# Kernel tuning notes

Measured on AMD Instinct MI355X. Metric: run time of the kernel, lower is better.

## Reference

```python
import jax, jax.numpy as jnp
import numpy as np
import math

D_MODEL = 768
N_HEADS = 12
HEAD_DIM = D_MODEL // N_HEADS
B, T = 2, 4096


def setup_inputs() -> dict:
    key = jax.random.key(0)
    k1, k2, k3, k4 = jax.random.split(key, 4)
    x = jax.random.normal(k1, (B, T, D_MODEL), dtype=jnp.float32)
    mask = jax.random.randint(k2, (B, T), 0, 2).astype(jnp.bool_)
    # torch Linear init scale ~ 1/sqrt(fan_in); use scaled normal for stability
    w_qkv = jax.random.normal(k3, (3 * D_MODEL, D_MODEL), dtype=jnp.float32) / math.sqrt(D_MODEL)
    w_proj = jax.random.normal(k4, (D_MODEL, D_MODEL), dtype=jnp.float32) / math.sqrt(D_MODEL)
    b_proj = jnp.zeros((D_MODEL,), dtype=jnp.float32)
    return {"x": x, "mask": mask, "w_qkv": w_qkv, "w_proj": w_proj, "b_proj": b_proj}


def reference(x, mask, w_qkv, w_proj, b_proj):
    Bb, Tt, D = x.shape
    H, Hd = N_HEADS, HEAD_DIM
    scale = math.sqrt(Hd)
    # qkv projection (bias-free): (B,T,3D) -> (3,B,H,T,Hd)
    qkv = jnp.einsum('btd,ed->bte', x, w_qkv)
    qkv = qkv.reshape(Bb, Tt, 3, H, Hd).transpose(2, 0, 3, 1, 4)
    q, k, v = qkv[0], qkv[1], qkv[2]
    # full T x T scores (faithful to non-fused original)
    attn = jnp.einsum('bhqd,bhkd->bhqk', q, k) / scale
    attn = jnp.where(mask[:, None, None, :], -jnp.inf, attn)
    attn = jax.nn.softmax(attn, axis=-1)  # dropout p=0 -> identity
    out = jnp.einsum('bhqk,bhkd->bhqd', attn, v)
    out = out.transpose(0, 2, 1, 3).reshape(Bb, Tt, D)
    return jnp.einsum('btd,ed->bte', out, w_proj) + b_proj
```

## Files before the change

### kernel.cpp

```cpp
#include <hip/hip_runtime.h>

#define D_MODEL 768
#define N_HEADS 12
#define SEQ 4096
#define KVB 64

typedef __attribute__((ext_vector_type(4))) float f32x4;
typedef __attribute__((ext_vector_type(16))) float f32x16;
typedef __attribute__((ext_vector_type(8))) short bf16x8;
typedef __attribute__((ext_vector_type(4))) unsigned short u16x4;

typedef __attribute__((address_space(3))) void lds_void;
typedef __attribute__((address_space(1))) const void glb_void;

static __device__ __forceinline__ void gld_lds16(const void* g, void* l) {
    __builtin_amdgcn_global_load_lds((glb_void*)g, (lds_void*)l, 16, 0, 0);
}

static __device__ __forceinline__ unsigned short f32_bf16(float f) {
    union { float f; unsigned int u; } c; c.f = f;
    unsigned int u = c.u;
    u += 0x7FFFu + ((u >> 16) & 1u);
    return (unsigned short)(u >> 16);
}

static __device__ __forceinline__ unsigned int cvtpk(float lo, float hi) {
    unsigned int r;
    asm("v_cvt_pk_bf16_f32 %0, %1, %2" : "=v"(r) : "v"(lo), "v"(hi));
    return r;
}

__global__ void cvt_bf16(const float* __restrict__ in, unsigned short* __restrict__ out, int n) {
    int i = (blockIdx.x * blockDim.x + threadIdx.x) * 4;
    int stride = gridDim.x * blockDim.x * 4;
    for (; i < n; i += stride) {
        f32x4 v = *(const f32x4*)(in + i);
        u16x4 o;
        o[0] = f32_bf16(v[0]); o[1] = f32_bf16(v[1]);
        o[2] = f32_bf16(v[2]); o[3] = f32_bf16(v[3]);
        *(u16x4*)(out + i) = o;
    }
}

#define QSCL 0.18033688f

__global__ __launch_bounds__(256) void qkv_gemm(const unsigned short* __restrict__ A,
                                                const unsigned short* __restrict__ Bw,
                                                unsigned short* __restrict__ qb,
                                                unsigned short* __restrict__ kb,
                                                unsigned short* __restrict__ vb) {
    __shared__ __attribute__((aligned(16))) unsigned short lA[128*32];
    __shared__ __attribute__((aligned(16))) unsigned short lB[128*32];
    const int K = 768;
    int tid = threadIdx.x;
    int wave = tid >> 6, lane = tid & 63;
    int qr = (wave >> 1) * 64, qc = (wave & 1) * 64;
    int m0 = blockIdx.x * 128, n0 = blockIdx.y * 128;
    f32x4 acc[4][4] = {};
    const int sl = (((lane >> 4) ^ (lane & 3)) * 16);

    for (int kt = 0; kt < K; kt += 32) {
        __syncthreads();
        #pragma unroll
        for (int i = 0; i < 2; ++i) {
            int c = i*256 + tid;
            int row = c >> 2;
            int col = ((c & 3) ^ (row & 3)) * 8;
            char* dA = (char*)lA + (i*256 + wave*64)*16;
            char* dB = (char*)lB + (i*256 + wave*64)*16;
            gld_lds16(A  + (size_t)(m0 + row) * K + kt + col, dA);
            gld_lds16(Bw + (size_t)(n0 + row) * K + kt + col, dB);
        }
        __syncthreads();
        bf16x8 af[4], bfr[4];
        #pragma unroll
        for (int m = 0; m < 4; ++m)
            af[m] = *(bf16x8*)((char*)lA + (qr + m*16 + (lane & 15))*64 + sl);
        #pragma unroll
        for (int n = 0; n < 4; ++n)
            bfr[n] = *(bf16x8*)((char*)lB + (qc + n*16 + (lane & 15))*64 + sl);
        #pragma unroll
        for (int m = 0; m < 4; ++m)
            #pragma unroll
            for (int n = 0; n < 4; ++n)
                acc[m][n] = __builtin_amdgcn_mfma_f32_16x16x32_bf16(af[m], bfr[n], acc[m][n], 0, 0, 0);
    }
    #pragma unroll
    for (int n = 0; n < 4; ++n) {
        int colg = n0 + qc + n*16 + (lane & 15);
        int s = colg / 768;
        int rem = colg - s * 768;
        int h = rem >> 6, d = rem & 63;
        if (s == 2) {
            #pragma unroll
            for (int m = 0; m < 4; ++m) {
                int rowb = m0 + qr + m*16 + (lane >> 4)*4;
                int bb = rowb >> 12, t0 = rowb & 4095;
                int t0p = (t0 & ~12) | ((t0 & 4) << 1) | ((t0 & 8) >> 1);
                u16x4 pk;
                #pragma unroll
                for (int r = 0; r < 4; ++r) pk[r] = f32_bf16(acc[m][n][r]);
                *(u16x4*)(vb + ((size_t)((bb*12 + h)*64 + d))*4096 + t0p) = pk;
            }
        } else {
            unsigned short* dst = (s == 0) ? qb : kb;
            float scl = (s == 0) ? QSCL : 1.0f;
            #pragma unroll
            for (int m = 0; m < 4; ++m) {
                int rowb = m0 + qr + m*16 + (lane >> 4)*4;
                #pragma unroll
                for (int r = 0; r < 4; ++r) {
                    int row = rowb + r;
                    int bb = row >> 12, t = row & 4095;
                    dst[((size_t)((bb*12 + h)*4096 + t))*64 + d] = f32_bf16(acc[m][n][r] * scl);
                }
            }
        }
    }
}

__global__ __launch_bounds__(512, 4) void attn_kern(const unsigned short* __restrict__ qbuf,
                                                    const unsigned short* __restrict__ kbuf,
                                                    const unsigned short* __restrict__ vtbuf,
                                                    const int* __restrict__ mask,
                                                    unsigned short* __restrict__ ob) {
    __shared__ __attribute__((aligned(16))) char lds[3][16384];
    __shared__ float lds_l[4][32];

    const int tid = threadIdx.x, wave = tid >> 6, lane = tid & 63;
    const int l31 = lane & 31, hi2 = lane >> 5;
    const int lane16 = lane * 16;
    const int wq = wave & 3, wk = wave >> 2;

    int raw = blockIdx.x;
    int sb = (raw & 7) * 96 + (raw >> 3);
    int bh = sb >> 5, qi = sb & 31;
    int q0 = qi * 128;
    int b = bh / 12, h = bh - b*12;

    const unsigned short* Qb = qbuf + (size_t)bh * SEQ * 64;
    const unsigned short* Kb = kbuf + (size_t)bh * SEQ * 64;
    const unsigned short* Vt = vtbuf + (size_t)bh * 64 * SEQ;
    const int* mrow = mask + b * SEQ + wk*32 + l31;

    bf16x8 bq[4];
    #pragma unroll
    for (int ds = 0; ds < 4; ++ds)
        bq[ds] = *(const bf16x8*)(Qb + (size_t)(q0 + wq*32 + l31)*64 + ds*16 + hi2*8);
    __builtin_amdgcn_sched_barrier(0);

    union U4 { unsigned int w[4]; bf16x8 v; };
    U4 bext; bext.w[0] = (hi2 == 0) ? 0x3F80u : 0u; bext.w[1] = bext.w[2] = bext.w[3] = 0u;

    auto stage = [&](char* buf, int kv0) {
        #pragma unroll
        for (int i = 0; i < 2; ++i) {
            int fi = wave*2 + i;
            const unsigned short* gsrc;
            if (fi < 8) {
                int kt = fi >> 2, ds = fi & 3;
                gsrc = Kb + (size_t)(kv0 + kt*32 + l31)*64 + ds*16 + hi2*8;
            } else {
                int g = fi - 8, dt = g >> 2, ks = g & 3;
                gsrc = Vt + (size_t)(dt*32 + l31)*4096 + kv0 + ks*16 + hi2*8;
            }
            gld_lds16(gsrc, buf + fi*1024);
        }
    };

    f32x16 oacc0 = {}, oacc1 = {};
    float lr = 0.0f;

    char* bA = lds[0];
    char* bB = lds[1];
    char* bC = lds[2];

    stage(bA, 0);
    int mb0 = mrow[0];
    stage(bB, KVB);
    int mb1 = mrow[KVB];
    asm volatile("s_waitcnt vmcnt(3)" ::: "memory");
    __builtin_amdgcn_sched_barrier(0);
    __builtin_amdgcn_s_barrier();
    __builtin_amdgcn_sched_barrier(0);

    const int NT = SEQ / KVB;
    for (int t = 0; t < NT; ++t) {
        int mb2 = 0;
        if (t + 2 < NT) {
            stage(bC, (t + 2) * KVB);
            mb2 = mrow[(t + 2) * KVB];
        }
        char* bufK = bA;
        char* bufV = bA + 8192;

        U4 ab;
        ab.w[0] = (hi2 == 0) ? (mb0 ? 0xC480u : 0xC18Au) : 0u;
        ab.w[1] = ab.w[2] = ab.w[3] = 0u;

        f32x16 s = {};
        s = __builtin_amdgcn_mfma_f32_32x32x16_bf16(ab.v, bext.v, s, 0, 0, 0);
        #pragma unroll
        for (int ds = 0; ds < 4; ++ds) {
            bf16x8 aK = *(bf16x8*)(bufK + (wk*4 + ds)*1024 + lane16);
            s = __builtin_amdgcn_mfma_f32_32x32x16_bf16(aK, bq[ds], s, 0, 0, 0);
        }

        float rs = 0.0f;
        #pragma unroll
        for (int i = 0; i < 16; ++i) { s[i] = __builtin_amdgcn_exp2f(s[i]); rs += s[i]; }
        rs += __shfl_xor(rs, 32);
        lr += rs;

        bf16x8 pa[2];
        #pragma unroll
        for (int ks = 0; ks < 2; ++ks) {
            U4 w;
            w.w[0] = cvtpk(s[8*ks+0], s[8*ks+1]);
            w.w[1] = cvtpk(s[8*ks+2], s[8*ks+3]);
            w.w[2] = cvtpk(s[8*ks+4], s[8*ks+5]);
            w.w[3] = cvtpk(s[8*ks+6], s[8*ks+7]);
            pa[ks] = w.v;
        }

        #pragma unroll
        for (int sb2 = 0; sb2 < 2; ++sb2) {
            int ksg = wk*2 + sb2;
            bf16x8 bv0 = *(bf16x8*)(bufV + (0*4 + ksg)*1024 + lane16);
            bf16x8 bv1 = *(bf16x8*)(bufV + (1*4 + ksg)*1024 + lane16);
            oacc0 = __builtin_amdgcn_mfma_f32_32x32x16_bf16(pa[sb2], bv0, oacc0, 0, 0, 0);
            oacc1 = __builtin_amdgcn_mfma_f32_32x32x16_bf16(pa[sb2], bv1, oacc1, 0, 0, 0);
        }

        if (t + 2 < NT) {
            asm volatile("s_waitcnt vmcnt(3)" ::: "memory");
        } else {
            asm volatile("s_waitcnt vmcnt(0)" ::: "memory");
        }
        __builtin_amdgcn_sched_barrier(0);
        __builtin_amdgcn_s_barrier();
        __builtin_amdgcn_sched_barrier(0);

        char* tmp = bA; bA = bB; bB = bC; bC = tmp;
        mb0 = mb1; mb1 = mb2;
    }

    float* cbase = (float*)lds + wq * 2048;
    if (wk == 1) {
        #pragma unroll
        for (int i = 0; i < 16; ++i) {
            cbase[i*64 + lane]        = oacc0[i];
            cbase[(16 + i)*64 + lane] = oacc1[i];
        }
        if (lane < 32) lds_l[wq][lane] = lr;
    }
    __syncthreads();
    if (wk == 0 && lane < 32) lds_l[wq][lane] += lr;
    __syncthreads();
    if (wk == 0) {
        #pragma unroll
        for (int r = 0; r < 16; ++r) {
            int q = (r & 3) + 8*(r >> 2) + 4*hi2;
            float inv = 1.0f / lds_l[wq][q];
            int tg = q0 + wq*32 + q;
            size_t base = ((size_t)(b*SEQ + tg)) * D_MODEL + h*64 + l31;
            ob[base]      = f32_bf16((oacc0[r] + cbase[r*64 + lane])        * inv);
            ob[base + 32] = f32_bf16((oacc1[r] + cbase[(16 + r)*64 + lane]) * inv);
        }
    }
}

__global__ __launch_bounds__(256) void proj_gemm(const unsigned short* __restrict__ A,
                                                 const unsigned short* __restrict__ Bw,
                                                 const float* __restrict__ bias,
                                                 float* __restrict__ out) {
    __shared__ __attribute__((aligned(16))) unsigned short lA[128*32];
    __shared__ __attribute__((aligned(16))) unsigned short lB[128*32];
    const int K = 768;
    int tid = threadIdx.x;
    int wave = tid >> 6, lane = tid & 63;
    int qr = (wave >> 1) * 64, qc = (wave & 1) * 64;
    int m0 = blockIdx.x * 128, n0 = blockIdx.y * 128;
    f32x4 acc[4][4] = {};
    const int sl = (((lane >> 4) ^ (lane & 3)) * 16);

    for (int kt = 0; kt < K; kt += 32) {
        __syncthreads();
        #pragma unroll
        for (int i = 0; i < 2; ++i) {
            int c = i*256 + tid;
            int row = c >> 2;
            int col = ((c & 3) ^ (row & 3)) * 8;
            char* dA = (char*)lA + (i*256 + wave*64)*16;
            char* dB = (char*)lB + (i*256 + wave*64)*16;
            gld_lds16(A  + (size_t)(m0 + row) * K + kt + col, dA);
            gld_lds16(Bw + (size_t)(n0 + row) * K + kt + col, dB);
        }
        __syncthreads();
        bf16x8 af[4], bfr[4];
        #pragma unroll
        for (int m = 0; m < 4; ++m)
            af[m] = *(bf16x8*)((char*)lA + (qr + m*16 + (lane & 15))*64 + sl);
        #pragma unroll
        for (int n = 0; n < 4; ++n)
            bfr[n] = *(bf16x8*)((char*)lB + (qc + n*16 + (lane & 15))*64 + sl);
        #pragma unroll
        for (int m = 0; m < 4; ++m)
            #pragma unroll
            for (int n = 0; n < 4; ++n)
                acc[m][n] = __builtin_amdgcn_mfma_f32_16x16x32_bf16(af[m], bfr[n], acc[m][n], 0, 0, 0);
    }
    #pragma unroll
    for (int n = 0; n < 4; ++n) {
        int colg = n0 + qc + n*16 + (lane & 15);
        float bn = bias[colg];
        #pragma unroll
        for (int m = 0; m < 4; ++m) {
            int rowb = m0 + qr + m*16 + (lane >> 4)*4;
            #pragma unroll
            for (int r = 0; r < 4; ++r)
                out[(size_t)(rowb + r) * 768 + colg] = acc[m][n][r] + bn;
        }
    }
}

extern "C" void kernel_launch(void* const* d_in, const int* in_sizes, int n_in,
                              void* d_out, int out_size, void* d_ws, size_t ws_size,
                              hipStream_t stream) {
    const float* x      = (const float*)d_in[0];
    const int*   mask   = (const int*)d_in[1];
    const float* w_qkv  = (const float*)d_in[2];
    const float* w_proj = (const float*)d_in[3];
    const float* b_proj = (const float*)d_in[4];
    float* out = (float*)d_out;

    unsigned short* ws = (unsigned short*)d_ws;
    unsigned short* xb     = ws;
    unsigned short* wqkvb  = xb     + 6291456;
    unsigned short* wprojb = wqkvb  + 1769472;
    unsigned short* qb     = wprojb + 589824;
    unsigned short* kb     = qb     + 6291456;
    unsigned short* vtb    = kb     + 6291456;
    unsigned short* ob     = vtb    + 6291456;

    cvt_bf16<<<1024, 256, 0, stream>>>(x,      xb,     6291456);
    cvt_bf16<<<256,  256, 0, stream>>>(w_qkv,  wqkvb,  1769472);
    cvt_bf16<<<128,  256, 0, stream>>>(w_proj, wprojb, 589824);

    qkv_gemm<<<dim3(64, 18), 256, 0, stream>>>(xb, wqkvb, qb, kb, vtb);
    attn_kern<<<768, 512, 0, stream>>>(qb, kb, vtb, mask, ob);
    proj_gemm<<<dim3(64, 6), 256, 0, stream>>>(ob, wprojb, b_proj, out);
}
```

Baseline: 239.3 us.

## Halve attention block waves, each wave processes two query tiles sharing K/V fragments

The attention kernel now runs 4 waves per block instead of 8. Each wave computes two 32-row query tiles, so every K and V fragment read from LDS feeds two MFMAs and LDS read traffic per unit of work is halved. The K/V staging pipeline goes from triple to double buffering with a full vmcnt(0) wait each iteration. Register pressure doubles (four output accumulators, two score tiles), and with only one tile prefetched ahead, load latency may be less well hidden.

```diff
diff --git a/kernel.cpp b/kernel.cpp
--- a/kernel.cpp
+++ b/kernel.cpp
@@ -119,18 +119,18 @@
     }
 }
 
-__global__ __launch_bounds__(512, 4) void attn_kern(const unsigned short* __restrict__ qbuf,
+__global__ __launch_bounds__(256, 2) void attn_kern(const unsigned short* __restrict__ qbuf,
                                                     const unsigned short* __restrict__ kbuf,
                                                     const unsigned short* __restrict__ vtbuf,
                                                     const int* __restrict__ mask,
                                                     unsigned short* __restrict__ ob) {
-    __shared__ __attribute__((aligned(16))) char lds[3][16384];
-    __shared__ float lds_l[4][32];
+    __shared__ __attribute__((aligned(16))) char lds[2][16384];
+    __shared__ float lds_l[2][2][32];
 
     const int tid = threadIdx.x, wave = tid >> 6, lane = tid & 63;
     const int l31 = lane & 31, hi2 = lane >> 5;
     const int lane16 = lane * 16;
-    const int wq = wave & 3, wk = wave >> 2;
+    const int wq = wave & 1, wk = wave >> 1;
 
     int raw = blockIdx.x;
     int sb = (raw & 7) * 96 + (raw >> 3);
@@ -143,10 +143,12 @@
     const unsigned short* Vt = vtbuf + (size_t)bh * 64 * SEQ;
     const int* mrow = mask + b * SEQ + wk*32 + l31;
 
-    bf16x8 bq[4];
+    bf16x8 bqA[4], bqB[4];
     #pragma unroll
-    for (int ds = 0; ds < 4; ++ds)
-        bq[ds] = *(const bf16x8*)(Qb + (size_t)(q0 + wq*32 + l31)*64 + ds*16 + hi2*8);
+    for (int ds = 0; ds < 4; ++ds) {
+        bqA[ds] = *(const bf16x8*)(Qb + (size_t)(q0 + wq*64 + l31)*64      + ds*16 + hi2*8);
+        bqB[ds] = *(const bf16x8*)(Qb + (size_t)(q0 + wq*64 + 32 + l31)*64 + ds*16 + hi2*8);
+    }
     __builtin_amdgcn_sched_barrier(0);
 
     union U4 { unsigned int w[4]; bf16x8 v; };
@@ -154,8 +156,8 @@
 
     auto stage = [&](char* buf, int kv0) {
         #pragma unroll
-        for (int i = 0; i < 2; ++i) {
-            int fi = wave*2 + i;
+        for (int i = 0; i < 4; ++i) {
+            int fi = wave*4 + i;
             const unsigned short* gsrc;
             if (fi < 8) {
                 int kt = fi >> 2, ds = fi & 3;
@@ -168,104 +170,127 @@
         }
     };
 
-    f32x16 oacc0 = {}, oacc1 = {};
-    float lr = 0.0f;
+    f32x16 accA0 = {}, accA1 = {}, accB0 = {}, accB1 = {};
+    float lrA = 0.0f, lrB = 0.0f;
 
     char* bA = lds[0];
     char* bB = lds[1];
-    char* bC = lds[2];
 
     stage(bA, 0);
     int mb0 = mrow[0];
-    stage(bB, KVB);
-    int mb1 = mrow[KVB];
-    asm volatile("s_waitcnt vmcnt(3)" ::: "memory");
+    asm volatile("s_waitcnt vmcnt(0)" ::: "memory");
     __builtin_amdgcn_sched_barrier(0);
     __builtin_amdgcn_s_barrier();
     __builtin_amdgcn_sched_barrier(0);
 
     const int NT = SEQ / KVB;
     for (int t = 0; t < NT; ++t) {
-        int mb2 = 0;
-        if (t + 2 < NT) {
-            stage(bC, (t + 2) * KVB);
-            mb2 = mrow[(t + 2) * KVB];
-        }
-        char* bufK = bA;
-        char* bufV = bA + 8192;
+        int mb1 = 0;
+        if (t + 1 < NT) {
+            stage(bB, (t + 1) * KVB);
+            mb1 = mrow[(t + 1) * KVB];
+        }
+        const char* bufK = bA;
+        const char* bufV = bA + 8192;
+
+        bf16x8 kf0 = *(const bf16x8*)(bufK + (wk*4 + 0)*1024 + lane16);
+        bf16x8 kf1 = *(const bf16x8*)(bufK + (wk*4 + 1)*1024 + lane16);
+        bf16x8 kf2 = *(const bf16x8*)(bufK + (wk*4 + 2)*1024 + lane16);
+        bf16x8 kf3 = *(const bf16x8*)(bufK + (wk*4 + 3)*1024 + lane16);
 
         U4 ab;
         ab.w[0] = (hi2 == 0) ? (mb0 ? 0xC480u : 0xC18Au) : 0u;
         ab.w[1] = ab.w[2] = ab.w[3] = 0u;
 
-        f32x16 s = {};
-        s = __builtin_amdgcn_mfma_f32_32x32x16_bf16(ab.v, bext.v, s, 0, 0, 0);
-        #pragma unroll
-        for (int ds = 0; ds < 4; ++ds) {
-            bf16x8 aK = *(bf16x8*)(bufK + (wk*4 + ds)*1024 + lane16);
-            s = __builtin_amdgcn_mfma_f32_32x32x16_bf16(aK, bq[ds], s, 0, 0, 0);
-        }
-
-        float rs = 0.0f;
-        #pragma unroll
-        for (int i = 0; i < 16; ++i) { s[i] = __builtin_amdgcn_exp2f(s[i]); rs += s[i]; }
-        rs += __shfl_xor(rs, 32);
-        lr += rs;
-
-        bf16x8 pa[2];
-        #pragma unroll
-        for (int ks = 0; ks < 2; ++ks) {
-            U4 w;
-            w.w[0] = cvtpk(s[8*ks+0], s[8*ks+1]);
-            w.w[1] = cvtpk(s[8*ks+2], s[8*ks+3]);
-            w.w[2] = cvtpk(s[8*ks+4], s[8*ks+5]);
-            w.w[3] = cvtpk(s[8*ks+6], s[8*ks+7]);
-            pa[ks] = w.v;
-        }
-
-        #pragma unroll
-        for (int sb2 = 0; sb2 < 2; ++sb2) {
-            int ksg = wk*2 + sb2;
-            bf16x8 bv0 = *(bf16x8*)(bufV + (0*4 + ksg)*1024 + lane16);
-            bf16x8 bv1 = *(bf16x8*)(bufV + (1*4 + ksg)*1024 + lane16);
-            oacc0 = __builtin_amdgcn_mfma_f32_32x32x16_bf16(pa[sb2], bv0, oacc0, 0, 0, 0);
-            oacc1 = __builtin_amdgcn_mfma_f32_32x32x16_bf16(pa[sb2], bv1, oacc1, 0, 0, 0);
-        }
-
-        if (t + 2 < NT) {
-            asm volatile("s_waitcnt vmcnt(3)" ::: "memory");
-        } else {
-            asm volatile("s_waitcnt vmcnt(0)" ::: "memory");
-        }
+        f32x16 sA = {}, sB = {};
+        sA = __builtin_amdgcn_mfma_f32_32x32x16_bf16(ab.v, bext.v, sA, 0, 0, 0);
+        sB = __builtin_amdgcn_mfma_f32_32x32x16_bf16(ab.v, bext.v, sB, 0, 0, 0);
+        sA = __builtin_amdgcn_mfma_f32_32x32x16_bf16(kf0, bqA[0], sA, 0, 0, 0);
+        sB = __builtin_amdgcn_mfma_f32_32x32x16_bf16(kf0, bqB[0], sB, 0, 0, 0);
+        sA = __builtin_amdgcn_mfma_f32_32x32x16_bf16(kf1, bqA[1], sA, 0, 0, 0);
+        sB = __builtin_amdgcn_mfma_f32_32x32x16_bf16(kf1, bqB[1], sB, 0, 0, 0);
+        sA = __builtin_amdgcn_mfma_f32_32x32x16_bf16(kf2, bqA[2], sA, 0, 0, 0);
+        sB = __builtin_amdgcn_mfma_f32_32x32x16_bf16(kf2, bqB[2], sB, 0, 0, 0);
+        sA = __builtin_amdgcn_mfma_f32_32x32x16_bf16(kf3, bqA[3], sA, 0, 0, 0);
+        sB = __builtin_amdgcn_mfma_f32_32x32x16_bf16(kf3, bqB[3], sB, 0, 0, 0);
+
+        bf16x8 vf00 = *(const bf16x8*)(bufV + (0*4 + wk*2 + 0)*1024 + lane16);
+        bf16x8 vf10 = *(const bf16x8*)(bufV + (1*4 + wk*2 + 0)*1024 + lane16);
+        bf16x8 vf01 = *(const bf16x8*)(bufV + (0*4 + wk*2 + 1)*1024 + lane16);
+        bf16x8 vf11 = *(const bf16x8*)(bufV + (1*4 + wk*2 + 1)*1024 + lane16);
+
+        {
+            float rs = 0.0f;
+            #pragma unroll
+            for (int i = 0; i < 16; ++i) { sA[i] = __builtin_amdgcn_exp2f(sA[i]); rs += sA[i]; }
+            rs += __shfl_xor(rs, 32);
+            lrA += rs;
+            U4 p0, p1;
+            p0.w[0] = cvtpk(sA[0], sA[1]);  p0.w[1] = cvtpk(sA[2], sA[3]);
+            p0.w[2] = cvtpk(sA[4], sA[5]);  p0.w[3] = cvtpk(sA[6], sA[7]);
+            p1.w[0] = cvtpk(sA[8], sA[9]);  p1.w[1] = cvtpk(sA[10], sA[11]);
+            p1.w[2] = cvtpk(sA[12], sA[13]); p1.w[3] = cvtpk(sA[14], sA[15]);
+            accA0 = __builtin_amdgcn_mfma_f32_32x32x16_bf16(p0.v, vf00, accA0, 0, 0, 0);
+            accA1 = __builtin_amdgcn_mfma_f32_32x32x16_bf16(p0.v, vf10, accA1, 0, 0, 0);
+            accA0 = __builtin_amdgcn_mfma_f32_32x32x16_bf16(p1.v, vf01, accA0, 0, 0, 0);
+            accA1 = __builtin_amdgcn_mfma_f32_32x32x16_bf16(p1.v, vf11, accA1, 0, 0, 0);
+        }
+        {
+            float rs = 0.0f;
+            #pragma unroll
+            for (int i = 0; i < 16; ++i) { sB[i] = __builtin_amdgcn_exp2f(sB[i]); rs += sB[i]; }
+            rs += __shfl_xor(rs, 32);
+            lrB += rs;
+            U4 p0, p1;
+            p0.w[0] = cvtpk(sB[0], sB[1]);  p0.w[1] = cvtpk(sB[2], sB[3]);
+            p0.w[2] = cvtpk(sB[4], sB[5]);  p0.w[3] = cvtpk(sB[6], sB[7]);
+            p1.w[0] = cvtpk(sB[8], sB[9]);  p1.w[1] = cvtpk(sB[10], sB[11]);
+            p1.w[2] = cvtpk(sB[12], sB[13]); p1.w[3] = cvtpk(sB[14], sB[15]);
+            accB0 = __builtin_amdgcn_mfma_f32_32x32x16_bf16(p0.v, vf00, accB0, 0, 0, 0);
+            accB1 = __builtin_amdgcn_mfma_f32_32x32x16_bf16(p0.v, vf10, accB1, 0, 0, 0);
+            accB0 = __builtin_amdgcn_mfma_f32_32x32x16_bf16(p1.v, vf01, accB0, 0, 0, 0);
+            accB1 = __builtin_amdgcn_mfma_f32_32x32x16_bf16(p1.v, vf11, accB1, 0, 0, 0);
+        }
+
+        asm volatile("s_waitcnt vmcnt(0)" ::: "memory");
         __builtin_amdgcn_sched_barrier(0);
         __builtin_amdgcn_s_barrier();
         __builtin_amdgcn_sched_barrier(0);
 
-        char* tmp = bA; bA = bB; bB = bC; bC = tmp;
-        mb0 = mb1; mb1 = mb2;
-    }
-
-    float* cbase = (float*)lds + wq * 2048;
+        char* tmp = bA; bA = bB; bB = tmp;
+        mb0 = mb1;
+    }
+
+    float* cbase = (float*)lds + wq * 4096;
     if (wk == 1) {
         #pragma unroll
         for (int i = 0; i < 16; ++i) {
-            cbase[i*64 + lane]        = oacc0[i];
-            cbase[(16 + i)*64 + lane] = oacc1[i];
-        }
-        if (lane < 32) lds_l[wq][lane] = lr;
+            cbase[(     i)*64 + lane] = accA0[i];
+            cbase[(16 + i)*64 + lane] = accA1[i];
+            cbase[(32 + i)*64 + lane] = accB0[i];
+            cbase[(48 + i)*64 + lane] = accB1[i];
+        }
+        if (lane < 32) { lds_l[wq][0][lane] = lrA; lds_l[wq][1][lane] = lrB; }
     }
     __syncthreads();
-    if (wk == 0 && lane < 32) lds_l[wq][lane] += lr;
+    if (wk == 0 && lane < 32) {
+        lds_l[wq][0][lane] += lrA;
+        lds_l[wq][1][lane] += lrB;
+    }
     __syncthreads();
     if (wk == 0) {
         #pragma unroll
         for (int r = 0; r < 16; ++r) {
             int q = (r & 3) + 8*(r >> 2) + 4*hi2;
-            float inv = 1.0f / lds_l[wq][q];
-            int tg = q0 + wq*32 + q;
-            size_t base = ((size_t)(b*SEQ + tg)) * D_MODEL + h*64 + l31;
-            ob[base]      = f32_bf16((oacc0[r] + cbase[r*64 + lane])        * inv);
-            ob[base + 32] = f32_bf16((oacc1[r] + cbase[(16 + r)*64 + lane]) * inv);
+            float invA = 1.0f / lds_l[wq][0][q];
+            float invB = 1.0f / lds_l[wq][1][q];
+            int tA = q0 + wq*64 + q;
+            size_t baseA = ((size_t)(b*SEQ + tA)) * D_MODEL + h*64 + l31;
+            size_t baseB = baseA + (size_t)32 * D_MODEL;
+            ob[baseA]      = f32_bf16((accA0[r] + cbase[(     r)*64 + lane]) * invA);
+            ob[baseA + 32] = f32_bf16((accA1[r] + cbase[(16 + r)*64 + lane]) * invA);
+            ob[baseB]      = f32_bf16((accB0[r] + cbase[(32 + r)*64 + lane]) * invB);
+            ob[baseB + 32] = f32_bf16((accB1[r] + cbase[(48 + r)*64 + lane]) * invB);
         }
     }
 }
@@ -348,6 +373,6 @@
     cvt_bf16<<<128,  256, 0, stream>>>(w_proj, wprojb, 589824);
 
     qkv_gemm<<<dim3(64, 18), 256, 0, stream>>>(xb, wqkvb, qb, kb, vtb);
-    attn_kern<<<768, 512, 0, stream>>>(qb, kb, vtb, mask, ob);
+    attn_kern<<<768, 256, 0, stream>>>(qb, kb, vtb, mask, ob);
     proj_gemm<<<dim3(64, 6), 256, 0, stream>>>(ob, wprojb, b_proj, out);
 }
```

Result: faster. 230.8 us (-3.6%).

## Double KV block to 128 with two-stage double buffering in attention

Applied to the files above, without the earlier changes.

Raises the KV tile size from 64 to 128 keys and switches from a triple-buffered ring with one-ahead-by-two prefetch to double buffering, so each barrier covers twice as much MFMA work and the loop runs half as many iterations. Each wave now computes two 32-key score tiles per iteration with independent accumulator chains, which gives the scheduler more parallel work. The cost is a full vmcnt(0) wait each iteration, since prefetch depth drops to one tile. It also keeps LDS at 64KB per block, which may affect occupancy alongside extra registers for the second score tile.

```diff
diff --git a/kernel.cpp b/kernel.cpp
--- a/kernel.cpp
+++ b/kernel.cpp
@@ -3,7 +3,7 @@
 #define D_MODEL 768
 #define N_HEADS 12
 #define SEQ 4096
-#define KVB 64
+#define KVB 128
 
 typedef __attribute__((ext_vector_type(4))) float f32x4;
 typedef __attribute__((ext_vector_type(16))) float f32x16;
@@ -124,7 +124,7 @@
                                                     const unsigned short* __restrict__ vtbuf,
                                                     const int* __restrict__ mask,
                                                     unsigned short* __restrict__ ob) {
-    __shared__ __attribute__((aligned(16))) char lds[3][16384];
+    __shared__ __attribute__((aligned(16))) char lds[2][32768];
     __shared__ float lds_l[4][32];
 
     const int tid = threadIdx.x, wave = tid >> 6, lane = tid & 63;
@@ -141,7 +141,7 @@
     const unsigned short* Qb = qbuf + (size_t)bh * SEQ * 64;
     const unsigned short* Kb = kbuf + (size_t)bh * SEQ * 64;
     const unsigned short* Vt = vtbuf + (size_t)bh * 64 * SEQ;
-    const int* mrow = mask + b * SEQ + wk*32 + l31;
+    const int* mrow = mask + b * SEQ + wk*64 + l31;
 
     bf16x8 bq[4];
     #pragma unroll
@@ -154,14 +154,14 @@
 
     auto stage = [&](char* buf, int kv0) {
         #pragma unroll
-        for (int i = 0; i < 2; ++i) {
-            int fi = wave*2 + i;
+        for (int i = 0; i < 4; ++i) {
+            int fi = wave*4 + i;
             const unsigned short* gsrc;
-            if (fi < 8) {
+            if (fi < 16) {
                 int kt = fi >> 2, ds = fi & 3;
                 gsrc = Kb + (size_t)(kv0 + kt*32 + l31)*64 + ds*16 + hi2*8;
             } else {
-                int g = fi - 8, dt = g >> 2, ks = g & 3;
+                int g = fi - 16, dt = g >> 3, ks = g & 7;
                 gsrc = Vt + (size_t)(dt*32 + l31)*4096 + kv0 + ks*16 + hi2*8;
             }
             gld_lds16(gsrc, buf + fi*1024);
@@ -173,76 +173,93 @@
 
     char* bA = lds[0];
     char* bB = lds[1];
-    char* bC = lds[2];
 
     stage(bA, 0);
-    int mb0 = mrow[0];
-    stage(bB, KVB);
-    int mb1 = mrow[KVB];
-    asm volatile("s_waitcnt vmcnt(3)" ::: "memory");
+    int mbl0 = mrow[0], mbh0 = mrow[32];
+    asm volatile("s_waitcnt vmcnt(0)" ::: "memory");
     __builtin_amdgcn_sched_barrier(0);
     __builtin_amdgcn_s_barrier();
     __builtin_amdgcn_sched_barrier(0);
 
     const int NT = SEQ / KVB;
     for (int t = 0; t < NT; ++t) {
-        int mb2 = 0;
-        if (t + 2 < NT) {
-            stage(bC, (t + 2) * KVB);
-            mb2 = mrow[(t + 2) * KVB];
-        }
-        char* bufK = bA;
-        char* bufV = bA + 8192;
-
-        U4 ab;
-        ab.w[0] = (hi2 == 0) ? (mb0 ? 0xC480u : 0xC18Au) : 0u;
-        ab.w[1] = ab.w[2] = ab.w[3] = 0u;
-
-        f32x16 s = {};
-        s = __builtin_amdgcn_mfma_f32_32x32x16_bf16(ab.v, bext.v, s, 0, 0, 0);
+        int mbl1 = 0, mbh1 = 0;
+        if (t + 1 < NT) {
+            stage(bB, (t + 1) * KVB);
+            mbl1 = mrow[(t + 1) * KVB];
+            mbh1 = mrow[(t + 1) * KVB + 32];
+        }
+        const char* bufK = bA;
+        const char* bufV = bA + 16384;
+        const int kt0 = wk*2, kt1 = wk*2 + 1;
+
+        U4 ab0, ab1;
+        ab0.w[0] = (hi2 == 0) ? (mbl0 ? 0xC480u : 0xC18Au) : 0u;
+        ab0.w[1] = ab0.w[2] = ab0.w[3] = 0u;
+        ab1.w[0] = (hi2 == 0) ? (mbh0 ? 0xC480u : 0xC18Au) : 0u;
+        ab1.w[1] = ab1.w[2] = ab1.w[3] = 0u;
+
+        f32x16 s0 = {}, s1 = {};
+        s0 = __builtin_amdgcn_mfma_f32_32x32x16_bf16(ab0.v, bext.v, s0, 0, 0, 0);
+        s1 = __builtin_amdgcn_mfma_f32_32x32x16_bf16(ab1.v, bext.v, s1, 0, 0, 0);
         #pragma unroll
         for (int ds = 0; ds < 4; ++ds) {
-            bf16x8 aK = *(bf16x8*)(bufK + (wk*4 + ds)*1024 + lane16);
-            s = __builtin_amdgcn_mfma_f32_32x32x16_bf16(aK, bq[ds], s, 0, 0, 0);
-        }
-
-        float rs = 0.0f;
-        #pragma unroll
-        for (int i = 0; i < 16; ++i) { s[i] = __builtin_amdgcn_exp2f(s[i]); rs += s[i]; }
-        rs += __shfl_xor(rs, 32);
-        lr += rs;
-
-        bf16x8 pa[2];
-        #pragma unroll
-        for (int ks = 0; ks < 2; ++ks) {
-            U4 w;
-            w.w[0] = cvtpk(s[8*ks+0], s[8*ks+1]);
-            w.w[1] = cvtpk(s[8*ks+2], s[8*ks+3]);
-            w.w[2] = cvtpk(s[8*ks+4], s[8*ks+5]);
-            w.w[3] = cvtpk(s[8*ks+6], s[8*ks+7]);
-            pa[ks] = w.v;
-        }
-
-        #pragma unroll
-        for (int sb2 = 0; sb2 < 2; ++sb2) {
-            int ksg = wk*2 + sb2;
-            bf16x8 bv0 = *(bf16x8*)(bufV + (0*4 + ksg)*1024 + lane16);
-            bf16x8 bv1 = *(bf16x8*)(bufV + (1*4 + ksg)*1024 + lane16);
-            oacc0 = __builtin_amdgcn_mfma_f32_32x32x16_bf16(pa[sb2], bv0, oacc0, 0, 0, 0);
-            oacc1 = __builtin_amdgcn_mfma_f32_32x32x16_bf16(pa[sb2], bv1, oacc1, 0, 0, 0);
-        }
-
-        if (t + 2 < NT) {
-            asm volatile("s_waitcnt vmcnt(3)" ::: "memory");
-        } else {
-            asm volatile("s_waitcnt vmcnt(0)" ::: "memory");
-        }
+            bf16x8 aK0 = *(const bf16x8*)(bufK + (kt0*4 + ds)*1024 + lane16);
+            bf16x8 aK1 = *(const bf16x8*)(bufK + (kt1*4 + ds)*1024 + lane16);
+            s0 = __builtin_amdgcn_mfma_f32_32x32x16_bf16(aK0, bq[ds], s0, 0, 0, 0);
+            s1 = __builtin_amdgcn_mfma_f32_32x32x16_bf16(aK1, bq[ds], s1, 0, 0, 0);
+        }
+
+        {
+            float rs = 0.0f;
+            #pragma unroll
+            for (int i = 0; i < 16; ++i) { s0[i] = __builtin_amdgcn_exp2f(s0[i]); rs += s0[i]; }
+            rs += __shfl_xor(rs, 32);
+            lr += rs;
+            U4 p0, p1;
+            p0.w[0] = cvtpk(s0[0], s0[1]);   p0.w[1] = cvtpk(s0[2], s0[3]);
+            p0.w[2] = cvtpk(s0[4], s0[5]);   p0.w[3] = cvtpk(s0[6], s0[7]);
+            p1.w[0] = cvtpk(s0[8], s0[9]);   p1.w[1] = cvtpk(s0[10], s0[11]);
+            p1.w[2] = cvtpk(s0[12], s0[13]); p1.w[3] = cvtpk(s0[14], s0[15]);
+            int ka = kt0*2, kb2 = kt0*2 + 1;
+            bf16x8 v00 = *(const bf16x8*)(bufV + (0*8 + ka)*1024 + lane16);
+            bf16x8 v10 = *(const bf16x8*)(bufV + (1*8 + ka)*1024 + lane16);
+            bf16x8 v01 = *(const bf16x8*)(bufV + (0*8 + kb2)*1024 + lane16);
+            bf16x8 v11 = *(const bf16x8*)(bufV + (1*8 + kb2)*1024 + lane16);
+            oacc0 = __builtin_amdgcn_mfma_f32_32x32x16_bf16(p0.v, v00, oacc0, 0, 0, 0);
+            oacc1 = __builtin_amdgcn_mfma_f32_32x32x16_bf16(p0.v, v10, oacc1, 0, 0, 0);
+            oacc0 = __builtin_amdgcn_mfma_f32_32x32x16_bf16(p1.v, v01, oacc0, 0, 0, 0);
+            oacc1 = __builtin_amdgcn_mfma_f32_32x32x16_bf16(p1.v, v11, oacc1, 0, 0, 0);
+        }
+        {
+            float rs = 0.0f;
+            #pragma unroll
+            for (int i = 0; i < 16; ++i) { s1[i] = __builtin_amdgcn_exp2f(s1[i]); rs += s1[i]; }
+            rs += __shfl_xor(rs, 32);
+            lr += rs;
+            U4 p0, p1;
+            p0.w[0] = cvtpk(s1[0], s1[1]);   p0.w[1] = cvtpk(s1[2], s1[3]);
+            p0.w[2] = cvtpk(s1[4], s1[5]);   p0.w[3] = cvtpk(s1[6], s1[7]);
+            p1.w[0] = cvtpk(s1[8], s1[9]);   p1.w[1] = cvtpk(s1[10], s1[11]);
+            p1.w[2] = cvtpk(s1[12], s1[13]); p1.w[3] = cvtpk(s1[14], s1[15]);
+            int ka = kt1*2, kb2 = kt1*2 + 1;
+            bf16x8 v00 = *(const bf16x8*)(bufV + (0*8 + ka)*1024 + lane16);
+            bf16x8 v10 = *(const bf16x8*)(bufV + (1*8 + ka)*1024 + lane16);
+            bf16x8 v01 = *(const bf16x8*)(bufV + (0*8 + kb2)*1024 + lane16);
+            bf16x8 v11 = *(const bf16x8*)(bufV + (1*8 + kb2)*1024 + lane16);
+            oacc0 = __builtin_amdgcn_mfma_f32_32x32x16_bf16(p0.v, v00, oacc0, 0, 0, 0);
+            oacc1 = __builtin_amdgcn_mfma_f32_32x32x16_bf16(p0.v, v10, oacc1, 0, 0, 0);
+            oacc0 = __builtin_amdgcn_mfma_f32_32x32x16_bf16(p1.v, v01, oacc0, 0, 0, 0);
+            oacc1 = __builtin_amdgcn_mfma_f32_32x32x16_bf16(p1.v, v11, oacc1, 0, 0, 0);
+        }
+
+        asm volatile("s_waitcnt vmcnt(0)" ::: "memory");
         __builtin_amdgcn_sched_barrier(0);
         __builtin_amdgcn_s_barrier();
         __builtin_amdgcn_sched_barrier(0);
 
-        char* tmp = bA; bA = bB; bB = bC; bC = tmp;
-        mb0 = mb1; mb1 = mb2;
+        char* tmp = bA; bA = bB; bB = tmp;
+        mbl0 = mbl1; mbh0 = mbh1;
     }
 
     float* cbase = (float*)lds + wq * 2048;
```

New measurement: 214.5 us (median of 3 runs). 1.12x faster.
